# Kernel optimization log

Hardware: AMD Instinct MI355X
Metric: run time of the kernel (lower is better)

Reference implementation:

```python
import jax, jax.numpy as jnp
import numpy as np

D = 1024

def setup_inputs() -> dict:
    key = jax.random.key(0)
    ks = jax.random.split(key, 7)
    s = 1.0 / np.sqrt(D)
    return {
        "x": jax.random.normal(ks[0], (8, 2048, D), dtype=jnp.float32),
        "Wq": jax.random.uniform(ks[1], (D, D), jnp.float32, -s, s),
        "bq": jax.random.uniform(ks[2], (D,), jnp.float32, -s, s),
        "Wk": jax.random.uniform(ks[3], (D, D), jnp.float32, -s, s),
        "bk": jax.random.uniform(ks[4], (D,), jnp.float32, -s, s),
        "Wv": jax.random.uniform(ks[5], (D, D), jnp.float32, -s, s),
        "bv": jax.random.uniform(ks[6], (D,), jnp.float32, -s, s),
    }

def reference(x, Wq, bq, Wk, bk, Wv, bv):
    # torch Linear: y = x @ W.T + b
    Q = jnp.einsum('bsd,ed->bse', x, Wq) + bq
    K = jnp.einsum('bsd,ed->bse', x, Wk) + bk
    V = jnp.einsum('bsd,ed->bse', x, Wv) + bv
    scores = jnp.einsum('bse,bte->bst', Q, K) / jnp.sqrt(jnp.float32(x.shape[-1]))
    weights = jax.nn.softmax(scores, axis=-1)
    out = jnp.einsum('bst,bte->bse', weights, V)
    return jnp.mean(out, axis=0)
```

## Files before the change

kernel.cpp:

```cpp
#include <hip/hip_runtime.h>

typedef unsigned short u16;
typedef __attribute__((ext_vector_type(8))) short s16x8;
typedef __attribute__((ext_vector_type(4))) short s16x4;
typedef __attribute__((ext_vector_type(4))) float f32x4;

typedef const __attribute__((address_space(1))) void gas_void;
typedef __attribute__((address_space(3))) void las_void;

__device__ inline u16 f2bf(float f){
  union { float f; unsigned u; } c; c.f = f;
  unsigned r = c.u + 0x7fffu + ((c.u >> 16) & 1u);
  return (u16)(r >> 16);
}
__device__ inline float bf2f(u16 b){
  union { unsigned u; float f; } c; c.u = ((unsigned)b) << 16;
  return c.f;
}

extern "C" __global__ __launch_bounds__(256) void cvt_f32_bf16(
    const float* __restrict__ src, u16* __restrict__ dst, int n4){
  int stride = gridDim.x * blockDim.x;
  for (int i = blockIdx.x * blockDim.x + threadIdx.x; i < n4; i += stride){
    float4 f = reinterpret_cast<const float4*>(src)[i];
    s16x4 o;
    o[0] = (short)f2bf(f.x); o[1] = (short)f2bf(f.y);
    o[2] = (short)f2bf(f.z); o[3] = (short)f2bf(f.w);
    reinterpret_cast<s16x4*>(dst)[i] = o;
  }
}

extern "C" __global__ __launch_bounds__(256) void cvt_w3(
    const float* __restrict__ w0, const float* __restrict__ w1,
    const float* __restrict__ w2, u16* __restrict__ dst, int n4each){
  int stride = gridDim.x * blockDim.x;
  int total = 3 * n4each;
  for (int i = blockIdx.x * blockDim.x + threadIdx.x; i < total; i += stride){
    int w = i / n4each, off = i - w * n4each;
    const float* src = w == 0 ? w0 : w == 1 ? w1 : w2;
    float4 f = reinterpret_cast<const float4*>(src)[off];
    s16x4 o;
    o[0] = (short)f2bf(f.x); o[1] = (short)f2bf(f.y);
    o[2] = (short)f2bf(f.z); o[3] = (short)f2bf(f.w);
    reinterpret_cast<s16x4*>(dst)[i] = o;
  }
}

extern "C" __global__ __launch_bounds__(256) void reduce8(
    const float* __restrict__ p, float* __restrict__ out, int n4, long stride4){
  int gs = gridDim.x * blockDim.x;
  for (int i = blockIdx.x * blockDim.x + threadIdx.x; i < n4; i += gs){
    float4 a = reinterpret_cast<const float4*>(p)[i];
    #pragma unroll
    for (int z = 1; z < 8; ++z){
      float4 b = reinterpret_cast<const float4*>(p)[i + z * stride4];
      a.x += b.x; a.y += b.y; a.z += b.z; a.w += b.w;
    }
    reinterpret_cast<float4*>(out)[i] = a;
  }
}

#define BM 256
#define BN 256
#define BK 64

__device__ inline void stage256(const u16* __restrict__ g, int ld, int row0, int k0,
                                u16* lds, int tid){
  const int wave = tid >> 6;
  #pragma unroll
  for (int j = 0; j < 4; ++j){
    int c = j * 512 + tid;
    int row = c >> 3, sch = c & 7;
    int ch = sch ^ (row & 7);
    const u16* src = g + (long)(row0 + row) * ld + k0 + ch * 8;
    u16* dst = lds + (size_t)(j * 512 + wave * 64) * 8;
    __builtin_amdgcn_global_load_lds((gas_void*)src, (las_void*)dst, 16, 0, 0);
  }
}

#define BARRIER() do { asm volatile("" ::: "memory"); \
                       __builtin_amdgcn_s_barrier();  \
                       asm volatile("" ::: "memory"); } while (0)

template<int EPI>
__global__ __launch_bounds__(512, 2) void gemm256(
    const u16* __restrict__ A, const u16* __restrict__ B, void* __restrict__ C,
    const float* __restrict__ bias, float scale, int K,
    int lda, int ldb, int ldc, long sAz, long sBz, long sCz)
{
  __shared__ u16 As[2][BM * BK];
  __shared__ u16 Bs[2][BN * BK];
  const int tid = threadIdx.x;
  const int lane = tid & 63, wave = tid >> 6;
  const int wm = (wave >> 2) * 128, wn = (wave & 3) * 64;

  const int gx = gridDim.x;
  const int nwg = gx * gridDim.y;
  const int hw = blockIdx.y * gx + blockIdx.x;
  const int lg = (hw & 7) * (nwg >> 3) + (hw >> 3);
  const int pr  = lg / (2 * gx);
  const int rem = lg - pr * 2 * gx;
  const int bm = (pr * 2 + (rem & 1)) * BM;
  const int bn = (rem >> 1) * BN;
  const int z = blockIdx.z;
  A += (long)z * sAz; B += (long)z * sBz;

  f32x4 acc[8][4];
  #pragma unroll
  for (int i = 0; i < 8; ++i)
    #pragma unroll
    for (int j = 0; j < 4; ++j) acc[i][j] = (f32x4){0.f, 0.f, 0.f, 0.f};

  const int lrow = lane & 15, lkg = lane >> 4;
  const int nt = K >> 6;

  auto lda4 = [&](s16x8* d, const u16* base, int ih, int kk){
    #pragma unroll
    for (int i = 0; i < 4; ++i){
      int row = wm + (ih * 4 + i) * 16 + lrow;
      int ch = (kk * 4 + lkg) ^ (row & 7);
      d[i] = *reinterpret_cast<const s16x8*>(
          reinterpret_cast<const char*>(base) + row * 128 + ch * 16);
    }
  };
  auto ldb4 = [&](s16x8* d, const u16* base, int kk){
    #pragma unroll
    for (int j = 0; j < 4; ++j){
      int row = wn + j * 16 + lrow;
      int ch = (kk * 4 + lkg) ^ (row & 7);
      d[j] = *reinterpret_cast<const s16x8*>(
          reinterpret_cast<const char*>(base) + row * 128 + ch * 16);
    }
  };

  #define MFMACL(AF, BF, RO)                                                   \
    _Pragma("unroll")                                                          \
    for (int i_ = 0; i_ < 4; ++i_)                                             \
      _Pragma("unroll")                                                        \
      for (int j_ = 0; j_ < 4; ++j_)                                           \
        acc[(RO) + i_][j_] = __builtin_amdgcn_mfma_f32_16x16x32_bf16(          \
            AF[i_], BF[j_], acc[(RO) + i_][j_], 0, 0, 0);

  stage256(A, lda, bm, 0, As[0], tid);
  stage256(B, ldb, bn, 0, Bs[0], tid);
  asm volatile("s_waitcnt vmcnt(0)" ::: "memory");
  BARRIER();

  for (int t = 0; t < nt; ++t){
    const int cur = t & 1, nxt = cur ^ 1;
    const bool pf = (t + 1) < nt;
    const int k1 = (t + 1) << 6;
    const u16* as = As[cur];
    const u16* bs = Bs[cur];
    s16x8 af0[4], af1[4], bfr0[4], bfr1[4];

    ldb4(bfr0, bs, 0);
    lda4(af0, as, 0, 0);
    lda4(af1, as, 1, 0);
    __builtin_amdgcn_s_setprio(1);
    MFMACL(af0, bfr0, 0);
    __builtin_amdgcn_s_setprio(0);
    ldb4(bfr1, bs, 1);
    lda4(af0, as, 0, 1);
    if (pf) stage256(A, lda, bm, k1, As[nxt], tid);
    __builtin_amdgcn_s_setprio(1);
    MFMACL(af1, bfr0, 4);
    __builtin_amdgcn_s_setprio(0);
    lda4(af1, as, 1, 1);
    if (pf) stage256(B, ldb, bn, k1, Bs[nxt], tid);
    __builtin_amdgcn_s_setprio(1);
    MFMACL(af0, bfr1, 0);
    MFMACL(af1, bfr1, 4);
    __builtin_amdgcn_s_setprio(0);

    asm volatile("s_waitcnt vmcnt(0)" ::: "memory");
    BARRIER();
  }

  #pragma unroll
  for (int i = 0; i < 8; ++i){
    #pragma unroll
    for (int j = 0; j < 4; ++j){
      #pragma unroll
      for (int r = 0; r < 4; ++r){
        int row = bm + wm + i * 16 + lkg * 4 + r;
        int col = bn + wn + j * 16 + lrow;
        float v = acc[i][j][r] * scale;
        if (EPI == 0){
          if (bias) v += bias[col];
          reinterpret_cast<u16*>(C)[(long)z * sCz + (long)row * ldc + col] = f2bf(v);
        } else if (EPI == 1){
          if (bias) v += bias[col];
          int b = row >> 11, tt = row & 2047;
          reinterpret_cast<u16*>(C)[((long)b << 21) + ((long)col << 11) + tt] = f2bf(v);
        } else {
          reinterpret_cast<float*>(C)[(long)z * sCz + (long)row * ldc + col] = v;
        }
      }
    }
  }
  #undef MFMACL
}

extern "C" __global__ __launch_bounds__(512) void softmax_rows_w(
    u16* __restrict__ S, int rows){
  const int lane = threadIdx.x & 63;
  const int gw = blockIdx.x * (blockDim.x >> 6) + (threadIdx.x >> 6);
  const int nw = gridDim.x * (blockDim.x >> 6);
  for (int row = gw; row < rows; row += nw){
    u16* p = S + (long)row * 2048;
    float v[32];
    float m = -3.4e38f;
    #pragma unroll
    for (int c = 0; c < 4; ++c){
      s16x8 vv = reinterpret_cast<const s16x8*>(p)[c * 64 + lane];
      #pragma unroll
      for (int j = 0; j < 8; ++j){
        float f = bf2f((u16)vv[c * 0 + j]);
        v[c * 8 + j] = f; m = fmaxf(m, f);
      }
    }
    #pragma unroll
    for (int o = 32; o; o >>= 1) m = fmaxf(m, __shfl_xor(m, o));
    float s = 0.f;
    #pragma unroll
    for (int j = 0; j < 32; ++j){ v[j] = __expf(v[j] - m); s += v[j]; }
    #pragma unroll
    for (int o = 32; o; o >>= 1) s += __shfl_xor(s, o);
    float inv = 1.0f / s;
    #pragma unroll
    for (int c = 0; c < 4; ++c){
      s16x8 ov;
      #pragma unroll
      for (int j = 0; j < 8; ++j) ov[j] = (short)f2bf(v[c * 8 + j] * inv);
      reinterpret_cast<s16x8*>(p)[c * 64 + lane] = ov;
    }
  }
}

extern "C" void kernel_launch(void* const* d_in, const int* in_sizes, int n_in,
                              void* d_out, int out_size, void* d_ws, size_t ws_size,
                              hipStream_t stream){
  const float* x  = (const float*)d_in[0];
  const float* Wq = (const float*)d_in[1];
  const float* bq = (const float*)d_in[2];
  const float* Wk = (const float*)d_in[3];
  const float* bk = (const float*)d_in[4];
  const float* Wv = (const float*)d_in[5];
  const float* bv = (const float*)d_in[6];

  const long NX = 16384L * 1024;
  const long NW = 1024L * 1024;
  const long NS = 8L * 2048 * 2048;

  u16* xbf = (u16*)d_ws;
  u16* Wb  = xbf + NX;
  u16* Qb  = Wb + 3 * NW;
  u16* Kb  = Qb + NX;
  u16* Vtb = Kb + NX;
  u16* S   = Vtb + NX;

  float* partial = (float*)Qb;

  size_t need = (size_t)(NX + 3 * NW + 3 * NX + NS) * 2;
  if (ws_size < need) return;

  cvt_f32_bf16<<<2048, 256, 0, stream>>>(x, xbf, (int)(NX / 4));
  cvt_w3<<<768, 256, 0, stream>>>(Wq, Wk, Wv, Wb, (int)(NW / 4));

  gemm256<0><<<dim3(4, 64, 1), 512, 0, stream>>>(
      xbf, Wb,          Qb,  bq, 1.f, 1024, 1024, 1024, 1024, 0, 0, 0);
  gemm256<0><<<dim3(4, 64, 1), 512, 0, stream>>>(
      xbf, Wb + NW,     Kb,  bk, 1.f, 1024, 1024, 1024, 1024, 0, 0, 0);
  gemm256<1><<<dim3(4, 64, 1), 512, 0, stream>>>(
      xbf, Wb + 2 * NW, Vtb, bv, 1.f, 1024, 1024, 1024, 0,    0, 0, 0);

  gemm256<0><<<dim3(8, 8, 8), 512, 0, stream>>>(
      Qb, Kb, S, nullptr, 0.03125f, 1024, 1024, 1024, 2048,
      2048L * 1024, 2048L * 1024, 2048L * 2048);

  softmax_rows_w<<<256, 512, 0, stream>>>(S, 8 * 2048);

  gemm256<2><<<dim3(4, 8, 8), 512, 0, stream>>>(
      S, Vtb, partial, nullptr, 0.125f, 2048, 2048, 2048, 1024,
      2048L * 2048, 1024L * 2048, 2048L * 1024);

  reduce8<<<1024, 256, 0, stream>>>(
      partial, (float*)d_out, (int)(2048L * 1024 / 4), 2048L * 1024 / 4);
}
```

Baseline: 339.3 us.

## Halve GEMM K-tile to 32, simplify pipeline, fuse QKV projections into one launch

```diff
diff --git a/kernel.cpp b/kernel.cpp
--- a/kernel.cpp
+++ b/kernel.cpp
@@ -62,16 +62,18 @@
 
 #define BM 256
 #define BN 256
-#define BK 64
+#define BK 32
+
+__device__ inline int swz(int row){ return (row & 3) ^ ((row >> 2) & 3); }
 
 __device__ inline void stage256(const u16* __restrict__ g, int ld, int row0, int k0,
                                 u16* lds, int tid){
   const int wave = tid >> 6;
   #pragma unroll
-  for (int j = 0; j < 4; ++j){
+  for (int j = 0; j < 2; ++j){
     int c = j * 512 + tid;
-    int row = c >> 3, sch = c & 7;
-    int ch = sch ^ (row & 7);
+    int row = c >> 2, sch = c & 3;
+    int ch = sch ^ swz(row);
     const u16* src = g + (long)(row0 + row) * ld + k0 + ch * 8;
     u16* dst = lds + (size_t)(j * 512 + wave * 64) * 8;
     __builtin_amdgcn_global_load_lds((gas_void*)src, (las_void*)dst, 16, 0, 0);
@@ -85,7 +87,8 @@
 template<int EPI>
 __global__ __launch_bounds__(512, 2) void gemm256(
     const u16* __restrict__ A, const u16* __restrict__ B, void* __restrict__ C,
-    const float* __restrict__ bias, float scale, int K,
+    const float* __restrict__ bias, const float* __restrict__ bias2,
+    const float* __restrict__ bias3, float scale, int K,
     int lda, int ldb, int ldc, long sAz, long sBz, long sCz)
 {
   __shared__ u16 As[2][BM * BK];
@@ -112,24 +115,24 @@
     for (int j = 0; j < 4; ++j) acc[i][j] = (f32x4){0.f, 0.f, 0.f, 0.f};
 
   const int lrow = lane & 15, lkg = lane >> 4;
-  const int nt = K >> 6;
-
-  auto lda4 = [&](s16x8* d, const u16* base, int ih, int kk){
+  const int nt = K >> 5;
+
+  auto lda4 = [&](s16x8* d, const u16* base, int ih){
     #pragma unroll
     for (int i = 0; i < 4; ++i){
       int row = wm + (ih * 4 + i) * 16 + lrow;
-      int ch = (kk * 4 + lkg) ^ (row & 7);
+      int ch = lkg ^ swz(row);
       d[i] = *reinterpret_cast<const s16x8*>(
-          reinterpret_cast<const char*>(base) + row * 128 + ch * 16);
+          reinterpret_cast<const char*>(base) + row * 64 + ch * 16);
     }
   };
-  auto ldb4 = [&](s16x8* d, const u16* base, int kk){
+  auto ldb4 = [&](s16x8* d, const u16* base){
     #pragma unroll
     for (int j = 0; j < 4; ++j){
       int row = wn + j * 16 + lrow;
-      int ch = (kk * 4 + lkg) ^ (row & 7);
+      int ch = lkg ^ swz(row);
       d[j] = *reinterpret_cast<const s16x8*>(
-          reinterpret_cast<const char*>(base) + row * 128 + ch * 16);
+          reinterpret_cast<const char*>(base) + row * 64 + ch * 16);
     }
   };
 
@@ -149,28 +152,21 @@
   for (int t = 0; t < nt; ++t){
     const int cur = t & 1, nxt = cur ^ 1;
     const bool pf = (t + 1) < nt;
-    const int k1 = (t + 1) << 6;
+    const int k1 = (t + 1) << 5;
     const u16* as = As[cur];
     const u16* bs = Bs[cur];
-    s16x8 af0[4], af1[4], bfr0[4], bfr1[4];
-
-    ldb4(bfr0, bs, 0);
-    lda4(af0, as, 0, 0);
-    lda4(af1, as, 1, 0);
+    s16x8 af0[4], af1[4], bfr[4];
+
+    if (pf){
+      stage256(A, lda, bm, k1, As[nxt], tid);
+      stage256(B, ldb, bn, k1, Bs[nxt], tid);
+    }
+    ldb4(bfr, bs);
+    lda4(af0, as, 0);
+    lda4(af1, as, 1);
     __builtin_amdgcn_s_setprio(1);
-    MFMACL(af0, bfr0, 0);
-    __builtin_amdgcn_s_setprio(0);
-    ldb4(bfr1, bs, 1);
-    lda4(af0, as, 0, 1);
-    if (pf) stage256(A, lda, bm, k1, As[nxt], tid);
-    __builtin_amdgcn_s_setprio(1);
-    MFMACL(af1, bfr0, 4);
-    __builtin_amdgcn_s_setprio(0);
-    lda4(af1, as, 1, 1);
-    if (pf) stage256(B, ldb, bn, k1, Bs[nxt], tid);
-    __builtin_amdgcn_s_setprio(1);
-    MFMACL(af0, bfr1, 0);
-    MFMACL(af1, bfr1, 4);
+    MFMACL(af0, bfr, 0);
+    MFMACL(af1, bfr, 4);
     __builtin_amdgcn_s_setprio(0);
 
     asm volatile("s_waitcnt vmcnt(0)" ::: "memory");
@@ -193,8 +189,18 @@
           if (bias) v += bias[col];
           int b = row >> 11, tt = row & 2047;
           reinterpret_cast<u16*>(C)[((long)b << 21) + ((long)col << 11) + tt] = f2bf(v);
+        } else if (EPI == 2){
+          reinterpret_cast<float*>(C)[(long)z * sCz + (long)row * ldc + col] = v;
         } else {
-          reinterpret_cast<float*>(C)[(long)z * sCz + (long)row * ldc + col] = v;
+          const long NXk = 16384L * 1024;
+          v += (z == 0 ? bias : z == 1 ? bias2 : bias3)[col];
+          u16* Cb = reinterpret_cast<u16*>(C);
+          if (z == 2){
+            int b = row >> 11, tt = row & 2047;
+            Cb[2 * NXk + ((long)b << 21) + ((long)col << 11) + tt] = f2bf(v);
+          } else {
+            Cb[(long)z * NXk + (long)row * ldc + col] = f2bf(v);
+          }
         }
       }
     }
@@ -216,7 +222,7 @@
       s16x8 vv = reinterpret_cast<const s16x8*>(p)[c * 64 + lane];
       #pragma unroll
       for (int j = 0; j < 8; ++j){
-        float f = bf2f((u16)vv[c * 0 + j]);
+        float f = bf2f((u16)vv[j]);
         v[c * 8 + j] = f; m = fmaxf(m, f);
       }
     }
@@ -268,21 +274,17 @@
   cvt_f32_bf16<<<2048, 256, 0, stream>>>(x, xbf, (int)(NX / 4));
   cvt_w3<<<768, 256, 0, stream>>>(Wq, Wk, Wv, Wb, (int)(NW / 4));
 
-  gemm256<0><<<dim3(4, 64, 1), 512, 0, stream>>>(
-      xbf, Wb,          Qb,  bq, 1.f, 1024, 1024, 1024, 1024, 0, 0, 0);
-  gemm256<0><<<dim3(4, 64, 1), 512, 0, stream>>>(
-      xbf, Wb + NW,     Kb,  bk, 1.f, 1024, 1024, 1024, 1024, 0, 0, 0);
-  gemm256<1><<<dim3(4, 64, 1), 512, 0, stream>>>(
-      xbf, Wb + 2 * NW, Vtb, bv, 1.f, 1024, 1024, 1024, 0,    0, 0, 0);
+  gemm256<3><<<dim3(4, 64, 3), 512, 0, stream>>>(
+      xbf, Wb, Qb, bq, bk, bv, 1.f, 1024, 1024, 1024, 1024, 0, NW, 0);
 
   gemm256<0><<<dim3(8, 8, 8), 512, 0, stream>>>(
-      Qb, Kb, S, nullptr, 0.03125f, 1024, 1024, 1024, 2048,
+      Qb, Kb, S, nullptr, nullptr, nullptr, 0.03125f, 1024, 1024, 1024, 2048,
       2048L * 1024, 2048L * 1024, 2048L * 2048);
 
   softmax_rows_w<<<256, 512, 0, stream>>>(S, 8 * 2048);
 
   gemm256<2><<<dim3(4, 8, 8), 512, 0, stream>>>(
-      S, Vtb, partial, nullptr, 0.125f, 2048, 2048, 2048, 1024,
+      S, Vtb, partial, nullptr, nullptr, nullptr, 0.125f, 2048, 2048, 2048, 1024,
       2048L * 2048, 1024L * 2048, 2048L * 1024);
 
   reduce8<<<1024, 256, 0, stream>>>(
```

Result: slower. 395.0 us (+16.4%).

## Fuse Q/K/V projections into one batched GEMM launch and issue prefetch earlier

Applied to the files above, without the earlier changes.

```diff
diff --git a/kernel.cpp b/kernel.cpp
--- a/kernel.cpp
+++ b/kernel.cpp
@@ -85,7 +85,8 @@
 template<int EPI>
 __global__ __launch_bounds__(512, 2) void gemm256(
     const u16* __restrict__ A, const u16* __restrict__ B, void* __restrict__ C,
-    const float* __restrict__ bias, float scale, int K,
+    const float* __restrict__ bias, const float* __restrict__ bias2,
+    const float* __restrict__ bias3, float scale, int K,
     int lda, int ldb, int ldc, long sAz, long sBz, long sCz)
 {
   __shared__ u16 As[2][BM * BK];
@@ -154,6 +155,10 @@
     const u16* bs = Bs[cur];
     s16x8 af0[4], af1[4], bfr0[4], bfr1[4];
 
+    if (pf){
+      stage256(A, lda, bm, k1, As[nxt], tid);
+      stage256(B, ldb, bn, k1, Bs[nxt], tid);
+    }
     ldb4(bfr0, bs, 0);
     lda4(af0, as, 0, 0);
     lda4(af1, as, 1, 0);
@@ -162,12 +167,10 @@
     __builtin_amdgcn_s_setprio(0);
     ldb4(bfr1, bs, 1);
     lda4(af0, as, 0, 1);
-    if (pf) stage256(A, lda, bm, k1, As[nxt], tid);
     __builtin_amdgcn_s_setprio(1);
     MFMACL(af1, bfr0, 4);
     __builtin_amdgcn_s_setprio(0);
     lda4(af1, as, 1, 1);
-    if (pf) stage256(B, ldb, bn, k1, Bs[nxt], tid);
     __builtin_amdgcn_s_setprio(1);
     MFMACL(af0, bfr1, 0);
     MFMACL(af1, bfr1, 4);
@@ -193,8 +196,18 @@
           if (bias) v += bias[col];
           int b = row >> 11, tt = row & 2047;
           reinterpret_cast<u16*>(C)[((long)b << 21) + ((long)col << 11) + tt] = f2bf(v);
+        } else if (EPI == 2){
+          reinterpret_cast<float*>(C)[(long)z * sCz + (long)row * ldc + col] = v;
         } else {
-          reinterpret_cast<float*>(C)[(long)z * sCz + (long)row * ldc + col] = v;
+          const long NXk = 16384L * 1024;
+          v += (z == 0 ? bias : z == 1 ? bias2 : bias3)[col];
+          u16* Cb = reinterpret_cast<u16*>(C);
+          if (z == 2){
+            int b = row >> 11, tt = row & 2047;
+            Cb[2 * NXk + ((long)b << 21) + ((long)col << 11) + tt] = f2bf(v);
+          } else {
+            Cb[(long)z * NXk + (long)row * ldc + col] = f2bf(v);
+          }
         }
       }
     }
@@ -216,7 +229,7 @@
       s16x8 vv = reinterpret_cast<const s16x8*>(p)[c * 64 + lane];
       #pragma unroll
       for (int j = 0; j < 8; ++j){
-        float f = bf2f((u16)vv[c * 0 + j]);
+        float f = bf2f((u16)vv[j]);
         v[c * 8 + j] = f; m = fmaxf(m, f);
       }
     }
@@ -268,21 +281,17 @@
   cvt_f32_bf16<<<2048, 256, 0, stream>>>(x, xbf, (int)(NX / 4));
   cvt_w3<<<768, 256, 0, stream>>>(Wq, Wk, Wv, Wb, (int)(NW / 4));
 
-  gemm256<0><<<dim3(4, 64, 1), 512, 0, stream>>>(
-      xbf, Wb,          Qb,  bq, 1.f, 1024, 1024, 1024, 1024, 0, 0, 0);
-  gemm256<0><<<dim3(4, 64, 1), 512, 0, stream>>>(
-      xbf, Wb + NW,     Kb,  bk, 1.f, 1024, 1024, 1024, 1024, 0, 0, 0);
-  gemm256<1><<<dim3(4, 64, 1), 512, 0, stream>>>(
-      xbf, Wb + 2 * NW, Vtb, bv, 1.f, 1024, 1024, 1024, 0,    0, 0, 0);
+  gemm256<3><<<dim3(4, 64, 3), 512, 0, stream>>>(
+      xbf, Wb, Qb, bq, bk, bv, 1.f, 1024, 1024, 1024, 1024, 0, NW, 0);
 
   gemm256<0><<<dim3(8, 8, 8), 512, 0, stream>>>(
-      Qb, Kb, S, nullptr, 0.03125f, 1024, 1024, 1024, 2048,
+      Qb, Kb, S, nullptr, nullptr, nullptr, 0.03125f, 1024, 1024, 1024, 2048,
       2048L * 1024, 2048L * 1024, 2048L * 2048);
 
   softmax_rows_w<<<256, 512, 0, stream>>>(S, 8 * 2048);
 
   gemm256<2><<<dim3(4, 8, 8), 512, 0, stream>>>(
-      S, Vtb, partial, nullptr, 0.125f, 2048, 2048, 2048, 1024,
+      S, Vtb, partial, nullptr, nullptr, nullptr, 0.125f, 2048, 2048, 2048, 1024,
       2048L * 2048, 1024L * 2048, 2048L * 1024);
 
   reduce8<<<1024, 256, 0, stream>>>(
```

Result: no change. 342.7 us (+1.0%).
